# Optimization experiments

Measured on AMD Instinct MI355X. Metric: run time of the kernel, lower is better.

The kernel has to match this reference:

```python
import jax, jax.numpy as jnp
import numpy as np


def setup_inputs() -> dict:
    key = jax.random.key(0)
    ks = jax.random.split(key, 6)
    B, S, I, H = 8, 4096, 512, 512
    scale = 1.0 / np.sqrt(I)
    return {
        "x": jax.random.normal(ks[0], (B, S, I), dtype=jnp.float32),
        "h_0": jax.random.normal(ks[1], (B, H), dtype=jnp.float32),
        "W_z": jax.random.normal(ks[2], (H, I), dtype=jnp.float32) * scale,
        "b_z": jax.random.normal(ks[3], (H,), dtype=jnp.float32) * scale,
        "W_h": jax.random.normal(ks[4], (H, I), dtype=jnp.float32) * scale,
        "b_h": jax.random.normal(ks[5], (H,), dtype=jnp.float32) * scale,
    }


def reference(x, h_0, W_z, b_z, W_h, b_h):
    # Gate and candidate projections (dense GEMMs over all timesteps at once)
    z = jax.nn.sigmoid(jnp.einsum("bsi,hi->bsh", x, W_z) + b_z)  # [B,S,H]
    h_tilde = jnp.einsum("bsi,hi->bsh", x, W_h) + b_h            # [B,S,H]

    # Linear recurrence h_t = a_t * h_{t-1} + b_t with a = 1-z, b = z*h_tilde.
    # Parallel associative scan over time; h_0 folded in as element 0 (a=1, b=h_0).
    a = jnp.concatenate([jnp.ones_like(h_0)[:, None, :], 1.0 - z], axis=1)     # [B,S+1,H]
    b = jnp.concatenate([h_0[:, None, :], z * h_tilde], axis=1)                # [B,S+1,H]

    def combine(c1, c2):
        a1, b1 = c1
        a2, b2 = c2
        return a1 * a2, a2 * b1 + b2

    _, h = jax.lax.associative_scan(combine, (a, b), axis=1)
    return h[:, 1:, :]  # drop the h_0 slot -> [B,S,H]
```

## Files before the change

### kernel.cpp

```cpp
#include <hip/hip_runtime.h>
#include <hip/hip_bf16.h>
#include <stdint.h>


typedef __attribute__((ext_vector_type(8))) short short8;
typedef __attribute__((ext_vector_type(4))) float f32x4;

#define AS1 __attribute__((address_space(1)))
#define AS3 __attribute__((address_space(3)))

__device__ inline void gload_lds16(const void* g, void* l) {
  __builtin_amdgcn_global_load_lds((AS1 uint32_t*)(g), (AS3 uint32_t*)(l), 16, 0, 0);
}

__device__ inline ushort f2bf(float f) {
  union { __hip_bfloat16 h; ushort u; } v;
  v.h = __float2bfloat16(f);
  return v.u;
}

__global__ void cvt_w(const float* __restrict__ wz, const float* __restrict__ wh,
                      ushort* __restrict__ wzb, ushort* __restrict__ whb) {
  int i = blockIdx.x * 256 + threadIdx.x;
  float4 a = reinterpret_cast<const float4*>(wz)[i];
  reinterpret_cast<ushort4*>(wzb)[i] =
      make_ushort4(f2bf(a.x), f2bf(a.y), f2bf(a.z), f2bf(a.w));
  float4 b = reinterpret_cast<const float4*>(wh)[i];
  reinterpret_cast<ushort4*>(whb)[i] =
      make_ushort4(f2bf(b.x), f2bf(b.y), f2bf(b.z), f2bf(b.w));
}

__global__ __launch_bounds__(256, 2) void gemm_gate(
    const float* __restrict__ x,
    const ushort* __restrict__ wzb,
    const ushort* __restrict__ whb,
    const float* __restrict__ b_z,
    const float* __restrict__ b_h,
    uint* __restrict__ ab,
    float2* __restrict__ ABc)
{
  __shared__ __align__(16) char smem[65536];

  const int t  = threadIdx.x;
  const int w  = t >> 6;
  const int l  = t & 63;
  const int lm = l & 15;
  const int lk = l >> 4;
  const int wm = w >> 1, wn = w & 1;
  const int bid  = blockIdx.x;
  const int tile = (bid & 7) * 128 + (bid >> 3);
  const int bx = tile >> 2;
  const int by = tile & 3;
  const int m0 = bx * 128;
  const int n0 = by * 128;

  const int srow = t >> 2;
  const int ssl  = t & 3;

  f32x4 acc[2][4][4];
  #pragma unroll
  for (int q = 0; q < 2; ++q)
    #pragma unroll
    for (int m = 0; m < 4; ++m)
      #pragma unroll
      for (int n = 0; n < 4; ++n)
        acc[q][m][n] = (f32x4){0.f, 0.f, 0.f, 0.f};

  auto stage = [&](int sel, int kt) {
    char* base = smem + sel * 32768;
    const int k0 = kt * 32;
    #pragma unroll
    for (int j = 0; j < 2; ++j) {
      int row  = j * 64 + srow;
      int sw   = (row >> 1) & 3;
      int qlog = ssl ^ sw;
      const float* xs = x + (size_t)(m0 + row) * 512 + k0 + qlog * 8;
      gload_lds16(xs,     base +        j * 4096 + w * 1024);
      gload_lds16(xs + 4, base + 8192 + j * 4096 + w * 1024);
      gload_lds16(wzb + (size_t)(n0 + row) * 512 + k0 + qlog * 8,
                  base + 16384 + j * 4096 + w * 1024);
      gload_lds16(whb + (size_t)(n0 + row) * 512 + k0 + qlog * 8,
                  base + 24576 + j * 4096 + w * 1024);
    }
  };

  stage(0, 0);

  #pragma unroll
  for (int kt = 0; kt < 16; ++kt) {
    const int sel = kt & 1;
    if (kt < 15) {
      stage(sel ^ 1, kt + 1);
      asm volatile("s_waitcnt vmcnt(8)" ::: "memory");
    } else {
      asm volatile("s_waitcnt vmcnt(0)" ::: "memory");
    }
    __builtin_amdgcn_s_barrier();

    const char* base = smem + sel * 32768;
    short8 af[4], bfz[4], bfh[4];
    #pragma unroll
    for (int m = 0; m < 4; ++m) {
      int row = wm * 64 + m * 16 + lm;
      int so  = ((lk ^ ((row >> 1) & 3)) << 4);
      f32x4 lo = *(const f32x4*)(base +        row * 64 + so);
      f32x4 hi = *(const f32x4*)(base + 8192 + row * 64 + so);
      short8 v;
      v[0] = (short)f2bf(lo[0]); v[1] = (short)f2bf(lo[1]);
      v[2] = (short)f2bf(lo[2]); v[3] = (short)f2bf(lo[3]);
      v[4] = (short)f2bf(hi[0]); v[5] = (short)f2bf(hi[1]);
      v[6] = (short)f2bf(hi[2]); v[7] = (short)f2bf(hi[3]);
      af[m] = v;
    }
    #pragma unroll
    for (int n = 0; n < 4; ++n) {
      int row = wn * 64 + n * 16 + lm;
      int so  = ((lk ^ ((row >> 1) & 3)) << 4);
      bfz[n] = *(const short8*)(base + 16384 + row * 64 + so);
      bfh[n] = *(const short8*)(base + 24576 + row * 64 + so);
    }
    __builtin_amdgcn_s_setprio(1);
    #pragma unroll
    for (int m = 0; m < 4; ++m)
      #pragma unroll
      for (int n = 0; n < 4; ++n) {
        acc[0][m][n] = __builtin_amdgcn_mfma_f32_16x16x32_bf16(af[m], bfz[n], acc[0][m][n], 0, 0, 0);
        acc[1][m][n] = __builtin_amdgcn_mfma_f32_16x16x32_bf16(af[m], bfh[n], acc[1][m][n], 0, 0, 0);
      }
    __builtin_amdgcn_s_setprio(0);
    __builtin_amdgcn_s_barrier();
  }

  #pragma unroll
  for (int n = 0; n < 4; ++n) {
    const int col = n0 + wn * 64 + n * 16 + lm;
    const float bzn = b_z[col];
    const float bhn = b_h[col];
    float av[4][4], bv[4][4];
    #pragma unroll
    for (int m = 0; m < 4; ++m) {
      #pragma unroll
      for (int j = 0; j < 4; ++j) {
        size_t grow = (size_t)(m0 + wm * 64 + m * 16 + lk * 4 + j);
        float uz = acc[0][m][n][j] + bzn;
        float uh = acc[1][m][n][j] + bhn;
        float z  = 1.f / (1.f + __expf(-uz));
        float a  = 1.f - z;
        float bb = z * uh;
        av[m][j] = a;
        bv[m][j] = bb;
        ab[grow * 512 + col] = (uint)f2bf(a) | ((uint)f2bf(bb) << 16);
      }
    }
    #pragma unroll
    for (int cb = 0; cb < 2; ++cb) {
      float At[2], Bt[2];
      #pragma unroll
      for (int mm = 0; mm < 2; ++mm) {
        float A = 1.f, Bv = 0.f;
        #pragma unroll
        for (int j = 0; j < 4; ++j) {
          float a = av[2 * cb + mm][j];
          float b = bv[2 * cb + mm][j];
          A  = a * A;
          Bv = a * Bv + b;
        }
        float Ag = 1.f, Bg = 0.f;
        #pragma unroll
        for (int q = 0; q < 4; ++q) {
          float Aq = __shfl(A,  lm + 16 * q);
          float Bq = __shfl(Bv, lm + 16 * q);
          Ag = Aq * Ag;
          Bg = Aq * Bg + Bq;
        }
        At[mm] = Ag;
        Bt[mm] = Bg;
      }
      float Achunk = At[1] * At[0];
      float Bchunk = At[1] * Bt[0] + Bt[1];
      if (lk == 0) {
        int bidx = bx >> 5;
        int c    = (bx & 31) * 4 + wm * 2 + cb;
        ABc[((size_t)bidx * 512 + col) * 128 + c] = make_float2(Achunk, Bchunk);
      }
    }
  }
}

__global__ __launch_bounds__(256) void chunk_scan(
    const float2* __restrict__ ABc,
    const float* __restrict__ h0,
    float* __restrict__ Hinit)
{
  __shared__ float sm[128][4];
  const int w = threadIdx.x >> 6, l = threadIdx.x & 63;
  const int b   = blockIdx.x & 7;
  const int h0g = (blockIdx.x >> 3) * 4;
  const int h   = h0g + w;

  const float2* base = ABc + ((size_t)b * 512 + h) * 128;
  float2 s1 = base[l];
  float2 s2 = base[64 + l];

  float A1 = s1.x, B1 = s1.y;
  #pragma unroll
  for (int d = 1; d < 64; d <<= 1) {
    float uA = __shfl_up(A1, d);
    float uB = __shfl_up(B1, d);
    if (l >= d) { B1 = A1 * uB + B1; A1 = A1 * uA; }
  }
  float A2 = s2.x, B2 = s2.y;
  #pragma unroll
  for (int d = 1; d < 64; d <<= 1) {
    float uA = __shfl_up(A2, d);
    float uB = __shfl_up(B2, d);
    if (l >= d) { B2 = A2 * uB + B2; A2 = A2 * uA; }
  }
  float PA = __shfl(A1, 63), PB = __shfl(B1, 63);
  float FA = A2 * PA;
  float FB = A2 * PB + B2;

  float e1A = __shfl_up(A1, 1), e1B = __shfl_up(B1, 1);
  if (l == 0) { e1A = 1.f; e1B = 0.f; }
  float e2A = __shfl_up(FA, 1), e2B = __shfl_up(FB, 1);
  if (l == 0) { e2A = PA; e2B = PB; }

  float h0v = h0[b * 512 + h];
  sm[l][w]      = e1A * h0v + e1B;
  sm[64 + l][w] = e2A * h0v + e2B;
  __syncthreads();

  const int tt = threadIdx.x;
  if (tt < 128) {
    float4 v = *(const float4*)sm[tt];
    *(float4*)(Hinit + ((size_t)b * 128 + tt) * 512 + h0g) = v;
  }
}

__global__ __launch_bounds__(256) void scan_write(
    const uint* __restrict__ ab,
    const float* __restrict__ Hinit,
    float* __restrict__ out)
{
  const int b   = blockIdx.x & 7;
  const int idx = (blockIdx.x >> 3) * 256 + threadIdx.x;
  const int cg  = idx & 127;
  const int c   = idx >> 7;
  const uint4* p = reinterpret_cast<const uint4*>(ab + ((size_t)(b * 4096 + c * 32)) * 512) + cg;
  float4 hv = *reinterpret_cast<const float4*>(Hinit + ((size_t)b * 128 + c) * 512 + cg * 4);
  f32x4* po = reinterpret_cast<f32x4*>(out + ((size_t)(b * 4096 + c * 32)) * 512 + cg * 4);
  uint4 u0 = p[0];
  uint4 u1 = p[128];
  uint4 u2 = p[256];
  #pragma unroll 4
  for (int t = 0; t < 32; ++t) {
    uint4 u = u0;
    u0 = u1; u1 = u2;
    if (t < 29) u2 = p[(size_t)(t + 3) * 128];
    hv.x = __uint_as_float(u.x << 16) * hv.x + __uint_as_float(u.x & 0xffff0000u);
    hv.y = __uint_as_float(u.y << 16) * hv.y + __uint_as_float(u.y & 0xffff0000u);
    hv.z = __uint_as_float(u.z << 16) * hv.z + __uint_as_float(u.z & 0xffff0000u);
    hv.w = __uint_as_float(u.w << 16) * hv.w + __uint_as_float(u.w & 0xffff0000u);
    f32x4 vv = {hv.x, hv.y, hv.z, hv.w};
    __builtin_nontemporal_store(vv, po + (size_t)t * 128);
  }
}

extern "C" void kernel_launch(void* const* d_in, const int* in_sizes, int n_in,
                              void* d_out, int out_size, void* d_ws, size_t ws_size,
                              hipStream_t stream) {
  const float* x   = (const float*)d_in[0];
  const float* h0  = (const float*)d_in[1];
  const float* W_z = (const float*)d_in[2];
  const float* b_z = (const float*)d_in[3];
  const float* W_h = (const float*)d_in[4];
  const float* b_h = (const float*)d_in[5];
  float* out = (float*)d_out;

  char* ws = (char*)d_ws;
  ushort* wzb   = (ushort*)(ws);
  ushort* whb   = (ushort*)(ws + 524288);
  uint*   ab    = (uint*)  (ws + 1048576);
  float2* ABc   = (float2*)(ws + 68157440);
  float*  Hinit = (float*) (ws + 72351744);

  cvt_w<<<256, 256, 0, stream>>>(W_z, W_h, wzb, whb);
  gemm_gate<<<1024, 256, 0, stream>>>(x, wzb, whb, b_z, b_h, ab, ABc);
  chunk_scan<<<1024, 256, 0, stream>>>(ABc, h0, Hinit);
  scan_write<<<512, 256, 0, stream>>>(ab, Hinit, out);
}
```

Before: 86.65 us.

## Fuse chunk-prefix scan into scan_write with redundant sequential carry computation

Removes the separate chunk_scan kernel and the Hinit buffer. Each scan_write block now serially folds the chunk carries for its column from chunk 0 up to its own chunk, using the ABc buffer transposed to [b][chunk][col] so these reads coalesce, and stages the entry states in shared memory. This saves one kernel launch and the Hinit round trip through global memory. In exchange it adds redundant serial work: late blocks walk up to 128 chunk steps, which lengthens the critical path of the write kernel, and the launch changes to 256 blocks of 512 threads.

```diff
diff --git a/kernel.cpp b/kernel.cpp
--- a/kernel.cpp
+++ b/kernel.cpp
@@ -181,88 +181,55 @@
       if (lk == 0) {
         int bidx = bx >> 5;
         int c    = (bx & 31) * 4 + wm * 2 + cb;
-        ABc[((size_t)bidx * 512 + col) * 128 + c] = make_float2(Achunk, Bchunk);
-      }
-    }
-  }
-}
-
-__global__ __launch_bounds__(256) void chunk_scan(
+        ABc[((size_t)bidx * 128 + c) * 512 + col] = make_float2(Achunk, Bchunk);
+      }
+    }
+  }
+}
+
+__global__ __launch_bounds__(512) void scan_write(
+    const uint* __restrict__ ab,
     const float2* __restrict__ ABc,
     const float* __restrict__ h0,
-    float* __restrict__ Hinit)
-{
-  __shared__ float sm[128][4];
-  const int w = threadIdx.x >> 6, l = threadIdx.x & 63;
-  const int b   = blockIdx.x & 7;
-  const int h0g = (blockIdx.x >> 3) * 4;
-  const int h   = h0g + w;
-
-  const float2* base = ABc + ((size_t)b * 512 + h) * 128;
-  float2 s1 = base[l];
-  float2 s2 = base[64 + l];
-
-  float A1 = s1.x, B1 = s1.y;
-  #pragma unroll
-  for (int d = 1; d < 64; d <<= 1) {
-    float uA = __shfl_up(A1, d);
-    float uB = __shfl_up(B1, d);
-    if (l >= d) { B1 = A1 * uB + B1; A1 = A1 * uA; }
-  }
-  float A2 = s2.x, B2 = s2.y;
-  #pragma unroll
-  for (int d = 1; d < 64; d <<= 1) {
-    float uA = __shfl_up(A2, d);
-    float uB = __shfl_up(B2, d);
-    if (l >= d) { B2 = A2 * uB + B2; A2 = A2 * uA; }
-  }
-  float PA = __shfl(A1, 63), PB = __shfl(B1, 63);
-  float FA = A2 * PA;
-  float FB = A2 * PB + B2;
-
-  float e1A = __shfl_up(A1, 1), e1B = __shfl_up(B1, 1);
-  if (l == 0) { e1A = 1.f; e1B = 0.f; }
-  float e2A = __shfl_up(FA, 1), e2B = __shfl_up(FB, 1);
-  if (l == 0) { e2A = PA; e2B = PB; }
-
-  float h0v = h0[b * 512 + h];
-  sm[l][w]      = e1A * h0v + e1B;
-  sm[64 + l][w] = e2A * h0v + e2B;
-  __syncthreads();
-
-  const int tt = threadIdx.x;
-  if (tt < 128) {
-    float4 v = *(const float4*)sm[tt];
-    *(float4*)(Hinit + ((size_t)b * 128 + tt) * 512 + h0g) = v;
-  }
-}
-
-__global__ __launch_bounds__(256) void scan_write(
-    const uint* __restrict__ ab,
-    const float* __restrict__ Hinit,
     float* __restrict__ out)
 {
-  const int b   = blockIdx.x & 7;
-  const int idx = (blockIdx.x >> 3) * 256 + threadIdx.x;
-  const int cg  = idx & 127;
-  const int c   = idx >> 7;
+  __shared__ float henter[4][512];
+  const int b    = blockIdx.x & 7;
+  const int c0   = (blockIdx.x >> 3) * 4;
+  const int t    = threadIdx.x;
+
+  {
+    const int h = t;
+    float hv = h0[b * 512 + h];
+    const float2* s = ABc + (size_t)b * 128 * 512 + h;
+    for (int j = 0; j < c0 + 4; ++j) {
+      if (j >= c0) henter[j - c0][h] = hv;
+      float2 ab2 = s[(size_t)j * 512];
+      hv = ab2.x * hv + ab2.y;
+    }
+  }
+  __syncthreads();
+
+  const int ci = t >> 7;
+  const int cg = t & 127;
+  const int c  = c0 + ci;
   const uint4* p = reinterpret_cast<const uint4*>(ab + ((size_t)(b * 4096 + c * 32)) * 512) + cg;
-  float4 hv = *reinterpret_cast<const float4*>(Hinit + ((size_t)b * 128 + c) * 512 + cg * 4);
+  float4 hv = *reinterpret_cast<const float4*>(&henter[ci][cg * 4]);
   f32x4* po = reinterpret_cast<f32x4*>(out + ((size_t)(b * 4096 + c * 32)) * 512 + cg * 4);
   uint4 u0 = p[0];
   uint4 u1 = p[128];
   uint4 u2 = p[256];
   #pragma unroll 4
-  for (int t = 0; t < 32; ++t) {
+  for (int tt = 0; tt < 32; ++tt) {
     uint4 u = u0;
     u0 = u1; u1 = u2;
-    if (t < 29) u2 = p[(size_t)(t + 3) * 128];
+    if (tt < 29) u2 = p[(size_t)(tt + 3) * 128];
     hv.x = __uint_as_float(u.x << 16) * hv.x + __uint_as_float(u.x & 0xffff0000u);
     hv.y = __uint_as_float(u.y << 16) * hv.y + __uint_as_float(u.y & 0xffff0000u);
     hv.z = __uint_as_float(u.z << 16) * hv.z + __uint_as_float(u.z & 0xffff0000u);
     hv.w = __uint_as_float(u.w << 16) * hv.w + __uint_as_float(u.w & 0xffff0000u);
     f32x4 vv = {hv.x, hv.y, hv.z, hv.w};
-    __builtin_nontemporal_store(vv, po + (size_t)t * 128);
+    __builtin_nontemporal_store(vv, po + (size_t)tt * 128);
   }
 }
 
@@ -282,10 +249,8 @@
   ushort* whb   = (ushort*)(ws + 524288);
   uint*   ab    = (uint*)  (ws + 1048576);
   float2* ABc   = (float2*)(ws + 68157440);
-  float*  Hinit = (float*) (ws + 72351744);
 
   cvt_w<<<256, 256, 0, stream>>>(W_z, W_h, wzb, whb);
   gemm_gate<<<1024, 256, 0, stream>>>(x, wzb, whb, b_z, b_h, ab, ABc);
-  chunk_scan<<<1024, 256, 0, stream>>>(ABc, h0, Hinit);
-  scan_write<<<512, 256, 0, stream>>>(ab, Hinit, out);
-}
+  scan_write<<<256, 512, 0, stream>>>(ab, ABc, h0, out);
+}
```

After: 105.2 us. 1.21x slower.
